# Performance work log

Hardware: AMD Instinct MI355X
Metric: run time of the kernel (lower is better)

The kernel has to match this reference:

```python
import jax, jax.numpy as jnp
import numpy as np
from jax import lax

DX = 1.0
DT = 0.01
NT = 1000  # T / dt = 10 / 0.01


def setup_inputs() -> dict:
    key = jax.random.key(0)
    u0 = jax.random.uniform(key, (64, 2048), dtype=jnp.float32)
    return {
        "u0": u0,
        "c": jnp.float32(1.0),
        "alpha": jnp.float32(1.0),
        "beta": jnp.float32(1.0),
    }


def reference(u0, c, alpha, beta):
    """Explicit-Euler finite-difference KS solver with periodic BCs:
        u_t = -c * u * u_x - alpha * u_xx - beta * u_xxxx
    Returns the full trajectory stacked over time: (NT+1, B, N)."""
    inv_2dx = 1.0 / (2.0 * DX)
    inv_dx2 = 1.0 / (DX * DX)
    inv_dx4 = 1.0 / (DX ** 4)

    def step(u, _):
        up1 = jnp.roll(u, -1, axis=-1)
        um1 = jnp.roll(u, 1, axis=-1)
        up2 = jnp.roll(u, -2, axis=-1)
        um2 = jnp.roll(u, 2, axis=-1)
        u_x = (up1 - um1) * inv_2dx
        u_xx = (up1 - 2.0 * u + um1) * inv_dx2
        u_xxxx = (up2 - 4.0 * up1 + 6.0 * u - 4.0 * um1 + um2) * inv_dx4
        u_new = u + DT * (-c * u * u_x - alpha * u_xx - beta * u_xxxx)
        return u_new, u_new

    _, traj = lax.scan(step, u0, None, length=NT)
    return jnp.concatenate([u0[None], traj], axis=0)  # (NT+1, B, N)
```

## Files before the change

### kernel.cpp

```cpp
#include <hip/hip_runtime.h>

#define NCOL  2048
#define NROW  64
#define NSTEP 1000
#define NTH   256
#define EPT   8

typedef float vf4 __attribute__((ext_vector_type(4)));
typedef float vf2 __attribute__((ext_vector_type(2)));

__global__ __launch_bounds__(NTH) void ks_kernel(
    const float* __restrict__ u0,
    const float* __restrict__ c_in,
    const float* __restrict__ alpha_in,
    const float* __restrict__ beta_in,
    float* __restrict__ out)
{
    __shared__ float buf[2][NCOL];

    const int row = blockIdx.x;
    const int tid = threadIdx.x;

    const float c     = c_in[0];
    const float alpha = alpha_in[0];
    const float beta  = beta_in[0];

    const float dt      = 0.01f;
    const float inv2dx  = 0.5f;
    const float invdx2  = 1.0f;
    const float invdx4  = 1.0f;

    const float* __restrict__ urow = u0 + (size_t)row * NCOL;
    vf4 v0 = ((const vf4*)urow)[tid * 2 + 0];
    vf4 v1 = ((const vf4*)urow)[tid * 2 + 1];
    ((vf4*)(buf[0]))[tid * 2 + 0] = v0;
    ((vf4*)(buf[0]))[tid * 2 + 1] = v1;

    float* __restrict__ orow0 = out + (size_t)row * NCOL;
    __builtin_nontemporal_store(v0, (vf4*)(orow0) + tid * 2 + 0);
    __builtin_nontemporal_store(v1, (vf4*)(orow0) + tid * 2 + 1);

    const int    base = tid * EPT;
    const size_t slab = (size_t)NROW * NCOL;
    float* outp = out + slab + (size_t)row * NCOL;

    int p = 0;
    vf4 pa, pb;
    float* pout = nullptr;

    for (int t = 1; t <= NSTEP; ++t) {
        __syncthreads();

        if (t > 1) {
            __builtin_nontemporal_store(pa, (vf4*)(pout));
            __builtin_nontemporal_store(pb, (vf4*)(pout) + 1);
        }

        const float* cur = buf[p];

        float w[12];
        #pragma unroll
        for (int i = 0; i < 6; ++i) {
            int idx = (base - 2 + 2 * i) & (NCOL - 1);
            vf2 pr = *(const vf2*)&cur[idx];
            w[2 * i]     = pr.x;
            w[2 * i + 1] = pr.y;
        }

        float nw[EPT];
        #pragma unroll
        for (int i = 0; i < EPT; ++i) {
            float um2 = w[i];
            float um1 = w[i + 1];
            float u   = w[i + 2];
            float up1 = w[i + 3];
            float up2 = w[i + 4];
            float u_x    = (up1 - um1) * inv2dx;
            float u_xx   = (up1 - 2.0f * u + um1) * invdx2;
            float u_xxxx = (up2 - 4.0f * up1 + 6.0f * u - 4.0f * um1 + um2) * invdx4;
            nw[i] = u + dt * (-c * u * u_x - alpha * u_xx - beta * u_xxxx);
        }

        float* nxt = buf[1 - p];
        vf4 na = { nw[0], nw[1], nw[2], nw[3] };
        vf4 nb = { nw[4], nw[5], nw[6], nw[7] };
        *(vf4*)&nxt[base]     = na;
        *(vf4*)&nxt[base + 4] = nb;

        pa   = na;
        pb   = nb;
        pout = outp + base;
        outp += slab;
        p ^= 1;
    }

    __builtin_nontemporal_store(pa, (vf4*)(pout));
    __builtin_nontemporal_store(pb, (vf4*)(pout) + 1);
}

extern "C" void kernel_launch(void* const* d_in, const int* in_sizes, int n_in,
                              void* d_out, int out_size, void* d_ws, size_t ws_size,
                              hipStream_t stream) {
    const float* u0    = (const float*)d_in[0];
    const float* c     = (const float*)d_in[1];
    const float* alpha = (const float*)d_in[2];
    const float* beta  = (const float*)d_in[3];
    float* out = (float*)d_out;

    ks_kernel<<<NROW, NTH, 0, stream>>>(u0, c, alpha, beta, out);
}
```

Baseline: 764.7 us.

## Split time steps across redundant blocks and keep state in registers with halo exchange

Launches four blocks per row. Each block recomputes the earlier time steps from u0 without storing them, then writes only its own quarter of the trajectory, which spreads the output store traffic over more CUs. The per-step full-row shared-memory buffer is replaced by register-resident values plus a small shared exchange of two-element halos, using a raw s_waitcnt/s_barrier. The cost is redundant compute, up to three quarters of the steps on the last segment's blocks. Results must stay bit-identical across blocks, which holds because the arithmetic is deterministic.

```diff
diff --git a/kernel.cpp b/kernel.cpp
--- a/kernel.cpp
+++ b/kernel.cpp
@@ -5,6 +5,8 @@
 #define NSTEP 1000
 #define NTH   256
 #define EPT   8
+#define NSEG  4
+#define SEGLEN (NSTEP / NSEG)
 
 typedef float vf4 __attribute__((ext_vector_type(4)));
 typedef float vf2 __attribute__((ext_vector_type(2)));
@@ -16,86 +18,79 @@
     const float* __restrict__ beta_in,
     float* __restrict__ out)
 {
-    __shared__ float buf[2][NCOL];
+    __shared__ vf2 xch[2][2][NTH];
 
-    const int row = blockIdx.x;
+    const int bid = blockIdx.x;
+    const int row = bid & (NROW - 1);
+    const int seg = bid >> 6;
     const int tid = threadIdx.x;
 
     const float c     = c_in[0];
     const float alpha = alpha_in[0];
     const float beta  = beta_in[0];
 
-    const float dt      = 0.01f;
-    const float inv2dx  = 0.5f;
-    const float invdx2  = 1.0f;
-    const float invdx4  = 1.0f;
+    const float dt     = 0.01f;
+    const float inv2dx = 0.5f;
+    const float invdx2 = 1.0f;
+    const float invdx4 = 1.0f;
 
     const float* __restrict__ urow = u0 + (size_t)row * NCOL;
-    vf4 v0 = ((const vf4*)urow)[tid * 2 + 0];
-    vf4 v1 = ((const vf4*)urow)[tid * 2 + 1];
-    ((vf4*)(buf[0]))[tid * 2 + 0] = v0;
-    ((vf4*)(buf[0]))[tid * 2 + 1] = v1;
+    vf4 a = ((const vf4*)urow)[tid * 2 + 0];
+    vf4 b = ((const vf4*)urow)[tid * 2 + 1];
+    float u[EPT] = {a.x, a.y, a.z, a.w, b.x, b.y, b.z, b.w};
 
-    float* __restrict__ orow0 = out + (size_t)row * NCOL;
-    __builtin_nontemporal_store(v0, (vf4*)(orow0) + tid * 2 + 0);
-    __builtin_nontemporal_store(v1, (vf4*)(orow0) + tid * 2 + 1);
-
-    const int    base = tid * EPT;
-    const size_t slab = (size_t)NROW * NCOL;
-    float* outp = out + slab + (size_t)row * NCOL;
+    if (seg == 0) {
+        float* orow0 = out + (size_t)row * NCOL + tid * EPT;
+        __builtin_nontemporal_store(a, (vf4*)orow0);
+        __builtin_nontemporal_store(b, (vf4*)orow0 + 1);
+    }
 
     int p = 0;
-    vf4 pa, pb;
-    float* pout = nullptr;
-
-    for (int t = 1; t <= NSTEP; ++t) {
-        __syncthreads();
-
-        if (t > 1) {
-            __builtin_nontemporal_store(pa, (vf4*)(pout));
-            __builtin_nontemporal_store(pb, (vf4*)(pout) + 1);
-        }
-
-        const float* cur = buf[p];
+    auto step = [&]() {
+        vf2 lo = {u[0], u[1]};
+        vf2 hi = {u[6], u[7]};
+        xch[p][0][tid] = lo;
+        xch[p][1][tid] = hi;
+        asm volatile("s_waitcnt lgkmcnt(0)\n\ts_barrier" ::: "memory");
+        vf2 L = xch[p][1][(tid - 1) & (NTH - 1)];
+        vf2 R = xch[p][0][(tid + 1) & (NTH - 1)];
 
         float w[12];
+        w[0] = L.x; w[1] = L.y;
         #pragma unroll
-        for (int i = 0; i < 6; ++i) {
-            int idx = (base - 2 + 2 * i) & (NCOL - 1);
-            vf2 pr = *(const vf2*)&cur[idx];
-            w[2 * i]     = pr.x;
-            w[2 * i + 1] = pr.y;
-        }
+        for (int i = 0; i < EPT; ++i) w[2 + i] = u[i];
+        w[10] = R.x; w[11] = R.y;
 
-        float nw[EPT];
+        constexpr int ord[EPT] = {2, 3, 4, 5, 0, 1, 6, 7};
         #pragma unroll
-        for (int i = 0; i < EPT; ++i) {
+        for (int k = 0; k < EPT; ++k) {
+            const int i = ord[k];
             float um2 = w[i];
             float um1 = w[i + 1];
-            float u   = w[i + 2];
+            float uc  = w[i + 2];
             float up1 = w[i + 3];
             float up2 = w[i + 4];
             float u_x    = (up1 - um1) * inv2dx;
-            float u_xx   = (up1 - 2.0f * u + um1) * invdx2;
-            float u_xxxx = (up2 - 4.0f * up1 + 6.0f * u - 4.0f * um1 + um2) * invdx4;
-            nw[i] = u + dt * (-c * u * u_x - alpha * u_xx - beta * u_xxxx);
+            float u_xx   = (up1 - 2.0f * uc + um1) * invdx2;
+            float u_xxxx = (up2 - 4.0f * up1 + 6.0f * uc - 4.0f * um1 + um2) * invdx4;
+            u[i] = uc + dt * (-c * uc * u_x - alpha * u_xx - beta * u_xxxx);
         }
+        p ^= 1;
+    };
 
-        float* nxt = buf[1 - p];
-        vf4 na = { nw[0], nw[1], nw[2], nw[3] };
-        vf4 nb = { nw[4], nw[5], nw[6], nw[7] };
-        *(vf4*)&nxt[base]     = na;
-        *(vf4*)&nxt[base + 4] = nb;
+    const int warm = seg * SEGLEN;
+    for (int t = 0; t < warm; ++t) step();
 
-        pa   = na;
-        pb   = nb;
-        pout = outp + base;
+    const size_t slab = (size_t)NROW * NCOL;
+    float* outp = out + (size_t)(warm + 1) * slab + (size_t)row * NCOL + tid * EPT;
+    for (int t = 0; t < SEGLEN; ++t) {
+        step();
+        vf4 na = {u[0], u[1], u[2], u[3]};
+        vf4 nb = {u[4], u[5], u[6], u[7]};
+        __builtin_nontemporal_store(na, (vf4*)outp);
+        __builtin_nontemporal_store(nb, (vf4*)outp + 1);
         outp += slab;
-        p ^= 1;
     }
-
-    __builtin_nontemporal_store(pa, (vf4*)(pout));
-    __builtin_nontemporal_store(pb, (vf4*)(pout) + 1);
 }
 
 extern "C" void kernel_launch(void* const* d_in, const int* in_sizes, int n_in,
@@ -107,5 +102,5 @@
     const float* beta  = (const float*)d_in[3];
     float* out = (float*)d_out;
 
-    ks_kernel<<<NROW, NTH, 0, stream>>>(u0, c, alpha, beta, out);
+    ks_kernel<<<NROW * NSEG, NTH, 0, stream>>>(u0, c, alpha, beta, out);
 }
```

New measurement: 742.8 us. 1.03x faster.
